# Kernel tuning notes

Measured on AMD Instinct MI355X. Metric: run time of the kernel, lower is better.

Reference implementation:

```python
import jax, jax.numpy as jnp
import numpy as np

BEV_H = 128; BEV_W = 128; HEADS = 8; POINTS = 4; NUM_LAYERS = 6
PC = (-51.2, -51.2, -5.0, 51.2, 51.2, 3.0)
EPS = 1e-5


def _layernorm(x, g, b):
    m = x.mean(-1, keepdims=True)
    v = x.var(-1, keepdims=True)
    return (x - m) * jax.lax.rsqrt(v + 1e-5) * g + b


def _bilinear(feat, loc):
    # feat: (H, W, D); loc: (..., 2) normalized xy in [0, 1]; zero padding outside.
    H, W = feat.shape[0], feat.shape[1]
    ix = loc[..., 0] * W - 0.5
    iy = loc[..., 1] * H - 0.5
    x0 = jnp.floor(ix); y0 = jnp.floor(iy)
    fx = ix - x0; fy = iy - y0
    out = 0.0
    for dx in (0, 1):
        for dy in (0, 1):
            xi = x0 + dx; yi = y0 + dy
            w = (fx if dx else 1.0 - fx) * (fy if dy else 1.0 - fy)
            m = (xi >= 0) & (xi < W) & (yi >= 0) & (yi < H)
            xi_c = jnp.clip(xi, 0, W - 1).astype(jnp.int32)
            yi_c = jnp.clip(yi, 0, H - 1).astype(jnp.int32)
            out = out + (w * m)[..., None] * feat[yi_c, xi_c]
    return out


def _deform_grid(q, value, H, W, ref, ow, ob, aw, ab):
    # Deformable attention over a (H, W) grid of values; q: (Nq, C), value: (H*W, C).
    Nq, C = q.shape
    hd = C // HEADS
    v = value.reshape(H, W, HEADS, hd).transpose(2, 0, 1, 3)            # (h, H, W, hd)
    off = (q @ ow + ob).reshape(Nq, HEADS, POINTS, 2)
    loc = ref[:, None, None, :] + off / jnp.array([W, H], q.dtype)      # (Nq, h, P, 2)
    attn = jax.nn.softmax((q @ aw + ab).reshape(Nq, HEADS, POINTS), axis=-1)
    sampled = jax.vmap(_bilinear)(v, loc.transpose(1, 0, 2, 3))         # (h, Nq, P, hd)
    return jnp.einsum('hnpd,nhp->nhd', sampled, attn).reshape(Nq, C)


def _sca(q, feats, ref_cam, valid, ow, ob, aw, ab):
    # Spatial cross-attention: feats (Ncam, h, Hf, Wf, hd), ref_cam (Ncam, Nq, P, 2),
    # valid (Ncam, Nq, P) float mask of in-frustum projections.
    Nq, C = q.shape
    Hf, Wf = feats.shape[2], feats.shape[3]
    off = (q @ ow + ob).reshape(Nq, HEADS, POINTS, 2)
    loc = ref_cam[:, None] + (off / jnp.array([Wf, Hf], q.dtype)).transpose(1, 0, 2, 3)[None]
    # loc: (Ncam, h, Nq, P, 2)
    attn = jax.nn.softmax((q @ aw + ab).reshape(Nq, HEADS, POINTS), axis=-1)
    sampled = jax.vmap(jax.vmap(_bilinear))(feats, loc)                 # (Ncam, h, Nq, P, hd)
    num = jnp.einsum('chnpd,nhp,cnp->nhd', sampled, attn, valid)
    cnt = jnp.maximum(valid.sum((0, 2)), 1.0)                           # (Nq,)
    return (num / cnt[:, None, None]).reshape(Nq, C)


def _forward(image_feats, camera_intrinsics, camera_extrinsics, prev_bev, bev_embed,
             tsa_vw, tsa_vb, tsa_ow, tsa_ob, tsa_aw, tsa_ab, tsa_pw, tsa_pb,
             sca_vw, sca_vb, sca_ow, sca_ob, sca_aw, sca_ab, sca_pw, sca_pb,
             ffn_w1, ffn_b1, ffn_w2, ffn_b2,
             ln1_g, ln1_b, ln2_g, ln2_b, ln3_g, ln3_b):
    Ncam, C, Hf, Wf = image_feats.shape
    hd = C // HEADS
    Nq = BEV_H * BEV_W
    dt = image_feats.dtype
    feats_flat = image_feats.transpose(0, 2, 3, 1).reshape(Ncam * Hf * Wf, C)

    # 2D reference points for temporal self-attention (each query's own cell).
    xs = (jnp.arange(BEV_W, dtype=dt) + 0.5) / BEV_W
    ys = (jnp.arange(BEV_H, dtype=dt) + 0.5) / BEV_H
    gx, gy = jnp.meshgrid(xs, ys)                                       # (H, W) each
    ref2d = jnp.stack([gx.reshape(-1), gy.reshape(-1)], -1)             # (Nq, 2)

    # 3D pillar reference points projected into each camera.
    xm = PC[0] + gx.reshape(-1) * (PC[3] - PC[0])
    ym = PC[1] + gy.reshape(-1) * (PC[4] - PC[1])
    zm = PC[2] + (jnp.arange(POINTS, dtype=dt) + 0.5) / POINTS * (PC[5] - PC[2])
    ref3d = jnp.stack([
        jnp.broadcast_to(xm[:, None], (Nq, POINTS)),
        jnp.broadcast_to(ym[:, None], (Nq, POINTS)),
        jnp.broadcast_to(zm[None, :], (Nq, POINTS)),
        jnp.ones((Nq, POINTS), dt)], -1)                                # (Nq, P, 4)
    ego2cam = jnp.linalg.inv(camera_extrinsics[0])                      # (Ncam, 4, 4)
    pcam = jnp.einsum('cij,npj->cnpi', ego2cam, ref3d)[..., :3]
    img = jnp.einsum('cij,cnpj->cnpi', camera_intrinsics[0], pcam)
    z = img[..., 2]
    un = img[..., 0] / (jnp.maximum(z, EPS) * Wf)
    vn = img[..., 1] / (jnp.maximum(z, EPS) * Hf)
    valid = ((z > EPS) & (un >= 0) & (un <= 1) & (vn >= 0) & (vn <= 1)).astype(dt)
    ref_cam = jnp.stack([un, vn], -1)                                   # (Ncam, Nq, P, 2)

    q = bev_embed                                                       # (Nq, C)
    prev = prev_bev[:, 0, :]                                            # (Nq, C), B = 1
    for l in range(NUM_LAYERS):
        # Temporal self-attention: deformable sampling from prev BEV + current BEV.
        v_prev = prev @ tsa_vw[l] + tsa_vb[l]
        v_cur = q @ tsa_vw[l] + tsa_vb[l]
        a = 0.5 * (_deform_grid(q, v_prev, BEV_H, BEV_W, ref2d, tsa_ow[l], tsa_ob[l], tsa_aw[l], tsa_ab[l])
                   + _deform_grid(q, v_cur, BEV_H, BEV_W, ref2d, tsa_ow[l], tsa_ob[l], tsa_aw[l], tsa_ab[l]))
        q = _layernorm(q + a @ tsa_pw[l] + tsa_pb[l], ln1_g[l], ln1_b[l])
        # Spatial cross-attention over multi-camera image features.
        v_img = (feats_flat @ sca_vw[l] + sca_vb[l]).reshape(Ncam, Hf, Wf, HEADS, hd).transpose(0, 3, 1, 2, 4)
        a = _sca(q, v_img, ref_cam, valid, sca_ow[l], sca_ob[l], sca_aw[l], sca_ab[l])
        q = _layernorm(q + a @ sca_pw[l] + sca_pb[l], ln2_g[l], ln2_b[l])
        # FFN
        a = jax.nn.relu(q @ ffn_w1[l] + ffn_b1[l]) @ ffn_w2[l] + ffn_b2[l]
        q = _layernorm(q + a, ln3_g[l], ln3_b[l])
    return q.T.reshape(1, C, BEV_H, BEV_W)


def setup_inputs() -> dict:
    key = jax.random.key(0)
    ks = iter(jax.random.split(key, 80))
    def nrm(shape, s=0.02):
        return jax.random.normal(next(ks), shape, jnp.float32) * s
    C, L, Ncam, Hf, Wf = 256, NUM_LAYERS, 6, 58, 100
    Nq = BEV_H * BEV_W
    HP, HP2 = HEADS * POINTS, HEADS * POINTS * 2
    # Structured nuScenes-like cameras: 6 yaws at 60 deg, intrinsics at feature-map scale.
    extr = np.zeros((1, Ncam, 4, 4), np.float32)
    for c in range(Ncam):
        t = c * np.pi / 3.0
        f = np.array([np.cos(t), np.sin(t), 0.0])
        xc = np.array([np.sin(t), -np.cos(t), 0.0])
        yc = np.array([0.0, 0.0, -1.0])
        extr[0, c, :3, :3] = np.stack([xc, yc, f], axis=1)
        extr[0, c, :3, 3] = 1.5 * f + np.array([0.0, 0.0, 1.5])
        extr[0, c, 3, 3] = 1.0
    intr = np.zeros((1, Ncam, 3, 3), np.float32)
    intr[0, :, 0, 0] = 80.0; intr[0, :, 1, 1] = 80.0
    intr[0, :, 0, 2] = Wf / 2.0; intr[0, :, 1, 2] = Hf / 2.0
    intr[0, :, 2, 2] = 1.0
    return {
        'image_feats': jax.random.normal(next(ks), (Ncam, C, Hf, Wf), jnp.float32),
        'camera_intrinsics': jnp.asarray(intr),
        'camera_extrinsics': jnp.asarray(extr),
        'prev_bev': jax.random.normal(next(ks), (Nq, 1, C), jnp.float32),
        'bev_embed': nrm((Nq, C)),
        'tsa_vw': nrm((L, C, C)), 'tsa_vb': jnp.zeros((L, C), jnp.float32),
        'tsa_ow': nrm((L, C, HP2)), 'tsa_ob': nrm((L, HP2), 2.0),
        'tsa_aw': nrm((L, C, HP)), 'tsa_ab': jnp.zeros((L, HP), jnp.float32),
        'tsa_pw': nrm((L, C, C)), 'tsa_pb': jnp.zeros((L, C), jnp.float32),
        'sca_vw': nrm((L, C, C)), 'sca_vb': jnp.zeros((L, C), jnp.float32),
        'sca_ow': nrm((L, C, HP2)), 'sca_ob': nrm((L, HP2), 2.0),
        'sca_aw': nrm((L, C, HP)), 'sca_ab': jnp.zeros((L, HP), jnp.float32),
        'sca_pw': nrm((L, C, C)), 'sca_pb': jnp.zeros((L, C), jnp.float32),
        'ffn_w1': nrm((L, C, 2 * C)), 'ffn_b1': jnp.zeros((L, 2 * C), jnp.float32),
        'ffn_w2': nrm((L, 2 * C, C)), 'ffn_b2': jnp.zeros((L, C), jnp.float32),
        'ln1_g': jnp.ones((L, C), jnp.float32), 'ln1_b': jnp.zeros((L, C), jnp.float32),
        'ln2_g': jnp.ones((L, C), jnp.float32), 'ln2_b': jnp.zeros((L, C), jnp.float32),
        'ln3_g': jnp.ones((L, C), jnp.float32), 'ln3_b': jnp.zeros((L, C), jnp.float32),
    }


def reference(image_feats, camera_intrinsics, camera_extrinsics, prev_bev, bev_embed,
              tsa_vw, tsa_vb, tsa_ow, tsa_ob, tsa_aw, tsa_ab, tsa_pw, tsa_pb,
              sca_vw, sca_vb, sca_ow, sca_ob, sca_aw, sca_ab, sca_pw, sca_pb,
              ffn_w1, ffn_b1, ffn_w2, ffn_b2,
              ln1_g, ln1_b, ln2_g, ln2_b, ln3_g, ln3_b):
    return _forward(image_feats, camera_intrinsics, camera_extrinsics, prev_bev, bev_embed,
                    tsa_vw, tsa_vb, tsa_ow, tsa_ob, tsa_aw, tsa_ab, tsa_pw, tsa_pb,
                    sca_vw, sca_vb, sca_ow, sca_ob, sca_aw, sca_ab, sca_pw, sca_pb,
                    ffn_w1, ffn_b1, ffn_w2, ffn_b2,
                    ln1_g, ln1_b, ln2_g, ln2_b, ln3_g, ln3_b)
```

## Files before the change

kernel.cpp:

```cpp
#include <hip/hip_runtime.h>
#include <hip/hip_bf16.h>
#include <math.h>

typedef __hip_bfloat16 bf16;

#define NQ      16384
#define CDIM    256
#define NHEADS  8
#define NPOINTS 4
#define NCAM    6
#define HF      58
#define WF      100
#define HWF     (HF*WF)
#define NFEAT   (NCAM*HWF)
#define HD      32
#define NLAYERS 6

typedef __attribute__((ext_vector_type(8))) short short8;
typedef __attribute__((ext_vector_type(4))) float floatx4;

__device__ __forceinline__ float toF(float x) { return x; }
__device__ __forceinline__ float toF(bf16 x) { return __bfloat162float(x); }
__device__ __forceinline__ void storeD(float* p, float v) { *p = v; }
__device__ __forceinline__ void storeD(bf16* p, float v) { *p = __float2bfloat16(v); }

__device__ __forceinline__ float bfLo(unsigned u) { return __uint_as_float(u << 16); }
__device__ __forceinline__ float bfHi(unsigned u) { return __uint_as_float(u & 0xffff0000u); }

__device__ __forceinline__ void gload_lds16(const bf16* g, bf16* l) {
    __builtin_amdgcn_global_load_lds(
        (const __attribute__((address_space(1))) void*)(g),
        (__attribute__((address_space(3))) void*)(l), 16, 0, 0);
}


template <typename DT, bool RELU, bool STAGE, bool ZF>
__global__ __launch_bounds__(256) void gemm_mfma(
    const bf16* __restrict__ A, const bf16* __restrict__ BT,
    const float* __restrict__ bias, DT* __restrict__ D,
    int M, int N, int K, size_t sB, size_t sBias, size_t sD)
{
    int z, bn, bm;
    if (ZF) {
        int nwg = gridDim.x;
        int logical = (blockIdx.x & 7) * (nwg >> 3) + (blockIdx.x >> 3);
        int idx = logical % (2 * NLAYERS);
        bm = (logical / (2 * NLAYERS)) * 128;
        z  = idx % NLAYERS;
        bn = (idx / NLAYERS) * 128;
    } else {
        z  = blockIdx.z;
        bn = blockIdx.x * 128;
        bm = blockIdx.y * 128;
    }
    BT += (size_t)z * sB;
    bias += (size_t)z * sBias;
    D += (size_t)z * sD;

    __shared__ bf16 smem[STAGE ? 128 * 136 : 128 * 64];
    bf16* As = smem;
    bf16* Bs = smem + 128 * 32;

    int tid = threadIdx.x;
    int lane = tid & 63, w = tid >> 6;
    int wm = w & 1, wn = w >> 1;
    int l15 = lane & 15, quad = lane >> 4;

    floatx4 acc[4][4];
#pragma unroll
    for (int i = 0; i < 4; i++)
#pragma unroll
        for (int j = 0; j < 4; j++)
            acc[i][j] = (floatx4){0.f, 0.f, 0.f, 0.f};

    int rsub = lane >> 2;
    int kc   = (((lane & 3) ^ ((rsub >> 1) & 3))) * 8;
    int sw   = (l15 >> 1) & 3;

    for (int k0 = 0; k0 < K; k0 += 32) {
#pragma unroll
        for (int h = 0; h < 2; h++) {
            int r0 = w * 32 + h * 16;
            int gm = bm + r0 + rsub;
            if (gm > M - 1) gm = M - 1;
            gload_lds16(A + (size_t)gm * K + k0 + kc, &As[r0 * 32]);
            gload_lds16(BT + (size_t)(bn + r0 + rsub) * K + k0 + kc, &Bs[r0 * 32]);
        }
        __syncthreads();

        short8 a[4], b[4];
#pragma unroll
        for (int i = 0; i < 4; i++)
            a[i] = *(const short8*)(&As[(wm * 64 + i * 16 + l15) * 32 + (quad ^ sw) * 8]);
#pragma unroll
        for (int j = 0; j < 4; j++)
            b[j] = *(const short8*)(&Bs[(wn * 64 + j * 16 + l15) * 32 + (quad ^ sw) * 8]);
#pragma unroll
        for (int i = 0; i < 4; i++)
#pragma unroll
            for (int j = 0; j < 4; j++)
                acc[i][j] = __builtin_amdgcn_mfma_f32_16x16x32_bf16(
                    a[i], b[j], acc[i][j], 0, 0, 0);
        __syncthreads();
    }

    if (STAGE) {
#pragma unroll
        for (int i = 0; i < 4; i++) {
#pragma unroll
            for (int j = 0; j < 4; j++) {
                int col = wn * 64 + j * 16 + l15;
                float bv = bias[bn + col];
#pragma unroll
                for (int r = 0; r < 4; r++) {
                    int row = wm * 64 + i * 16 + quad * 4 + r;
                    float v = acc[i][j][r] + bv;
                    if (RELU) v = fmaxf(v, 0.f);
                    smem[row * 136 + col] = __float2bfloat16(v);
                }
            }
        }
        __syncthreads();
        int lr0 = tid >> 4;
        int ck  = tid & 15;
#pragma unroll
        for (int pass = 0; pass < 8; pass++) {
            int lr = pass * 16 + lr0;
            int gm = bm + lr;
            if (gm < M) {
                uint4 v = *(const uint4*)(&smem[lr * 136 + ck * 8]);
                *(uint4*)((bf16*)D + (size_t)gm * N + bn + ck * 8) = v;
            }
        }
    } else {
#pragma unroll
        for (int i = 0; i < 4; i++) {
#pragma unroll
            for (int j = 0; j < 4; j++) {
                int col = bn + wn * 64 + j * 16 + l15;
                float bv = bias[col];
#pragma unroll
                for (int r = 0; r < 4; r++) {
                    int row = bm + wm * 64 + i * 16 + quad * 4 + r;
                    if (row < M) {
                        float v = acc[i][j][r] + bv;
                        if (RELU) v = fmaxf(v, 0.f);
                        storeD(&D[(size_t)row * N + col], v);
                    }
                }
            }
        }
    }
}

__global__ __launch_bounds__(256) void gemm_off(
    const bf16* __restrict__ A, const bf16* __restrict__ BT,
    const float* __restrict__ bias, float* __restrict__ D)
{
    __shared__ bf16 As[64 * 32];
    __shared__ bf16 Bs[64 * 32];

    int tid = threadIdx.x;
    int lane = tid & 63, w = tid >> 6;
    int l15 = lane & 15, quad = lane >> 4;
    int bm = blockIdx.y * 64, bn = blockIdx.x * 64;

    floatx4 acc[4];
#pragma unroll
    for (int j = 0; j < 4; j++)
        acc[j] = (floatx4){0.f, 0.f, 0.f, 0.f};

    int rsub = lane >> 2;
    int kc   = (((lane & 3) ^ ((rsub >> 1) & 3))) * 8;
    int sw   = (l15 >> 1) & 3;

    for (int k0 = 0; k0 < 256; k0 += 32) {
        gload_lds16(A + (size_t)(bm + w * 16 + rsub) * 256 + k0 + kc, &As[w * 16 * 32]);
        gload_lds16(BT + (size_t)(bn + w * 16 + rsub) * 256 + k0 + kc, &Bs[w * 16 * 32]);
        __syncthreads();

        short8 a = *(const short8*)(&As[(w * 16 + l15) * 32 + (quad ^ sw) * 8]);
        short8 b[4];
#pragma unroll
        for (int j = 0; j < 4; j++)
            b[j] = *(const short8*)(&Bs[(j * 16 + l15) * 32 + (quad ^ sw) * 8]);
#pragma unroll
        for (int j = 0; j < 4; j++)
            acc[j] = __builtin_amdgcn_mfma_f32_16x16x32_bf16(a, b[j], acc[j], 0, 0, 0);
        __syncthreads();
    }

#pragma unroll
    for (int j = 0; j < 4; j++) {
        int col = bn + j * 16 + l15;
        float bv = bias[col];
#pragma unroll
        for (int r = 0; r < 4; r++) {
            int row = bm + w * 16 + quad * 4 + r;
            D[(size_t)row * 128 + col] = acc[j][r] + bv;
        }
    }
}

__global__ __launch_bounds__(256) void gemm_tsa(
    const bf16* __restrict__ qmean, const bf16* __restrict__ qb,
    const bf16* __restrict__ BT, const float* __restrict__ bias,
    bf16* __restrict__ vgrid, float* __restrict__ offlog)
{
    int bn3 = blockIdx.x;
    int bm = blockIdx.y * 128;
    int bn = bn3 * 128;
    const bf16* A = (bn3 == 2) ? qb : qmean;

    __shared__ bf16 smem[128 * 136];
    bf16* As = smem;
    bf16* Bs = smem + 128 * 32;

    int tid = threadIdx.x;
    int lane = tid & 63, w = tid >> 6;
    int wm = w & 1, wn = w >> 1;
    int l15 = lane & 15, quad = lane >> 4;

    floatx4 acc[4][4];
#pragma unroll
    for (int i = 0; i < 4; i++)
#pragma unroll
        for (int j = 0; j < 4; j++)
            acc[i][j] = (floatx4){0.f, 0.f, 0.f, 0.f};

    int rsub = lane >> 2;
    int kc   = (((lane & 3) ^ ((rsub >> 1) & 3))) * 8;
    int sw   = (l15 >> 1) & 3;

    for (int k0 = 0; k0 < 256; k0 += 32) {
#pragma unroll
        for (int h = 0; h < 2; h++) {
            int r0 = w * 32 + h * 16;
            gload_lds16(A + (size_t)(bm + r0 + rsub) * 256 + k0 + kc, &As[r0 * 32]);
            gload_lds16(BT + (size_t)(bn + r0 + rsub) * 256 + k0 + kc, &Bs[r0 * 32]);
        }
        __syncthreads();

        short8 a[4], b[4];
#pragma unroll
        for (int i = 0; i < 4; i++)
            a[i] = *(const short8*)(&As[(wm * 64 + i * 16 + l15) * 32 + (quad ^ sw) * 8]);
#pragma unroll
        for (int j = 0; j < 4; j++)
            b[j] = *(const short8*)(&Bs[(wn * 64 + j * 16 + l15) * 32 + (quad ^ sw) * 8]);
#pragma unroll
        for (int i = 0; i < 4; i++)
#pragma unroll
            for (int j = 0; j < 4; j++)
                acc[i][j] = __builtin_amdgcn_mfma_f32_16x16x32_bf16(
                    a[i], b[j], acc[i][j], 0, 0, 0);
        __syncthreads();
    }

    if (bn3 < 2) {
#pragma unroll
        for (int i = 0; i < 4; i++) {
#pragma unroll
            for (int j = 0; j < 4; j++) {
                int col = wn * 64 + j * 16 + l15;
                float bv = bias[bn + col];
#pragma unroll
                for (int r = 0; r < 4; r++) {
                    int row = wm * 64 + i * 16 + quad * 4 + r;
                    smem[row * 136 + col] = __float2bfloat16(acc[i][j][r] + bv);
                }
            }
        }
        __syncthreads();
        int lr0 = tid >> 4;
        int ck  = tid & 15;
#pragma unroll
        for (int pass = 0; pass < 8; pass++) {
            int lr = pass * 16 + lr0;
            uint4 v = *(const uint4*)(&smem[lr * 136 + ck * 8]);
            *(uint4*)(vgrid + (size_t)(bm + lr) * 256 + bn + ck * 8) = v;
        }
    } else {
#pragma unroll
        for (int i = 0; i < 4; i++) {
#pragma unroll
            for (int j = 0; j < 4; j++) {
                int col = wn * 64 + j * 16 + l15;
                float bv = bias[256 + col];
#pragma unroll
                for (int r = 0; r < 4; r++) {
                    int row = bm + wm * 64 + i * 16 + quad * 4 + r;
                    offlog[(size_t)row * 128 + col] = acc[i][j][r] + bv;
                }
            }
        }
    }
}

template <bool QM>
__global__ __launch_bounds__(512) void gemm_ln(
    const bf16* __restrict__ A, const bf16* __restrict__ BT,
    const float* __restrict__ bias,
    bf16* __restrict__ qb,
    const float* __restrict__ g, const float* __restrict__ b,
    int K, const bf16* __restrict__ prevb, bf16* __restrict__ qmean)
{
    __shared__ bf16 As[64 * 32];
    __shared__ bf16 Bs[256 * 32];
    __shared__ float red[2][64][4];
    __shared__ float stats[2][64];

    int tid = threadIdx.x;
    int lane = tid & 63, w = tid >> 6;
    int wm = w & 1, wn = w >> 1;
    int l15 = lane & 15, quad = lane >> 4;
    int bm = blockIdx.x * 64;

    floatx4 acc[2][4];
#pragma unroll
    for (int i = 0; i < 2; i++)
#pragma unroll
        for (int j = 0; j < 4; j++)
            acc[i][j] = (floatx4){0.f, 0.f, 0.f, 0.f};

    int rsub = lane >> 2;
    int kc   = (((lane & 3) ^ ((rsub >> 1) & 3))) * 8;
    int sw   = (l15 >> 1) & 3;

    for (int k0 = 0; k0 < K; k0 += 32) {
#pragma unroll
        for (int h = 0; h < 2; h++) {
            int r0 = w * 32 + h * 16;
            gload_lds16(BT + (size_t)(r0 + rsub) * K + k0 + kc, &Bs[r0 * 32]);
        }
        if (w < 4)
            gload_lds16(A + (size_t)(bm + w * 16 + rsub) * K + k0 + kc,
                        &As[w * 16 * 32]);
        __syncthreads();

        short8 a[2], bfr[4];
#pragma unroll
        for (int i = 0; i < 2; i++)
            a[i] = *(const short8*)(&As[(wm * 32 + i * 16 + l15) * 32 + (quad ^ sw) * 8]);
#pragma unroll
        for (int j = 0; j < 4; j++)
            bfr[j] = *(const short8*)(&Bs[(wn * 64 + j * 16 + l15) * 32 + (quad ^ sw) * 8]);
#pragma unroll
        for (int i = 0; i < 2; i++)
#pragma unroll
            for (int j = 0; j < 4; j++)
                acc[i][j] = __builtin_amdgcn_mfma_f32_16x16x32_bf16(
                    a[i], bfr[j], acc[i][j], 0, 0, 0);
        __syncthreads();
    }

    float x[2][4][4];
#pragma unroll
    for (int i = 0; i < 2; i++) {
#pragma unroll
        for (int j = 0; j < 4; j++) {
            int col = wn * 64 + j * 16 + l15;
            float bv = bias[col];
#pragma unroll
            for (int r = 0; r < 4; r++) {
                int row = bm + wm * 32 + i * 16 + quad * 4 + r;
                x[i][j][r] = toF(qb[(size_t)row * CDIM + col]) + acc[i][j][r] + bv;
            }
        }
    }
#pragma unroll
    for (int i = 0; i < 2; i++) {
#pragma unroll
        for (int r = 0; r < 4; r++) {
            float s = x[i][0][r] + x[i][1][r] + x[i][2][r] + x[i][3][r];
            float sq = x[i][0][r] * x[i][0][r] + x[i][1][r] * x[i][1][r] +
                       x[i][2][r] * x[i][2][r] + x[i][3][r] * x[i][3][r];
#pragma unroll
            for (int m = 1; m < 16; m <<= 1) {
                s += __shfl_xor(s, m);
                sq += __shfl_xor(sq, m);
            }
            if (l15 == 0) {
                int rl = wm * 32 + i * 16 + quad * 4 + r;
                red[0][rl][wn] = s;
                red[1][rl][wn] = sq;
            }
        }
    }
    __syncthreads();
    if (tid < 64) {
        float s = red[0][tid][0] + red[0][tid][1] + red[0][tid][2] + red[0][tid][3];
        float sq = red[1][tid][0] + red[1][tid][1] + red[1][tid][2] + red[1][tid][3];
        float mean = s * (1.f / CDIM);
        float var = fmaxf(sq * (1.f / CDIM) - mean * mean, 0.f);
        stats[0][tid] = mean;
        stats[1][tid] = rsqrtf(var + 1e-5f);
    }
    __syncthreads();
#pragma unroll
    for (int i = 0; i < 2; i++) {
#pragma unroll
        for (int j = 0; j < 4; j++) {
            int col = wn * 64 + j * 16 + l15;
            float gc = g[col], bc = b[col];
#pragma unroll
            for (int r = 0; r < 4; r++) {
                int rl = wm * 32 + i * 16 + quad * 4 + r;
                int row = bm + rl;
                float y = (x[i][j][r] - stats[0][rl]) * stats[1][rl] * gc + bc;
                qb[(size_t)row * CDIM + col] = __float2bfloat16(y);
                if (QM)
                    qmean[(size_t)row * CDIM + col] = __float2bfloat16(
                        0.5f * (toF(prevb[(size_t)row * CDIM + col]) + y));
            }
        }
    }
}

__global__ __launch_bounds__(256) void qmean_kernel(
    const bf16* __restrict__ a, const bf16* __restrict__ b, bf16* __restrict__ o)
{
    int i = blockIdx.x * 256 + threadIdx.x;
    short8 va = ((const short8*)a)[i];
    short8 vb = ((const short8*)b)[i];
    short8 vo;
#pragma unroll
    for (int j = 0; j < 8; j++) {
        float fa = __uint_as_float(((unsigned)(unsigned short)va[j]) << 16);
        float fb = __uint_as_float(((unsigned)(unsigned short)vb[j]) << 16);
        union { bf16 h; short s; } u;
        u.h = __float2bfloat16(0.5f * (fa + fb));
        vo[j] = u.s;
    }
    ((short8*)o)[i] = vo;
}

__global__ void wt_cvt_kernel(const float* __restrict__ W, bf16* __restrict__ WT,
                              int K, int N)
{
    __shared__ float tile[32][33];
    int l = blockIdx.z;
    const float* Wl = W + (size_t)l * K * N;
    bf16* WTl = WT + (size_t)l * K * N;
    int k0 = blockIdx.x * 32, n0 = blockIdx.y * 32;
    int tx = threadIdx.x, ty = threadIdx.y;
    for (int i = 0; i < 32; i += 8)
        tile[ty + i][tx] = Wl[(size_t)(k0 + ty + i) * N + n0 + tx];
    __syncthreads();
    for (int i = 0; i < 32; i += 8)
        WTl[(size_t)(n0 + ty + i) * K + k0 + tx] = __float2bfloat16(tile[tx][ty + i]);
}

__global__ void pack_tsa_kernel(const float* __restrict__ vw, const float* __restrict__ vb,
                                const float* __restrict__ ow, const float* __restrict__ ob,
                                const float* __restrict__ aw, const float* __restrict__ ab,
                                bf16* __restrict__ WT, float* __restrict__ BIAS)
{
    int n = blockIdx.x;
    int l = blockIdx.y;
    int k = threadIdx.x;
    float v = 0.f;
    if (n < 256)      v = vw[((size_t)l * 256 + k) * 256 + n];
    else if (n < 320) v = ow[((size_t)l * 256 + k) * 64 + (n - 256)];
    else if (n < 352) v = aw[((size_t)l * 256 + k) * 32 + (n - 320)];
    WT[((size_t)l * 384 + n) * 256 + k] = __float2bfloat16(v);
    if (k == 0) {
        float bv = 0.f;
        if (n < 256)      bv = vb[l * 256 + n];
        else if (n < 320) bv = ob[l * 64 + (n - 256)];
        else if (n < 352) bv = ab[l * 32 + (n - 320)];
        BIAS[l * 384 + n] = bv;
    }
}

__global__ void pack_offattn_kernel(const float* __restrict__ ow, const float* __restrict__ ob,
                                    const float* __restrict__ aw, const float* __restrict__ ab,
                                    bf16* __restrict__ WT, float* __restrict__ BIAS)
{
    int l = blockIdx.y;
    int n = blockIdx.x;
    int k = threadIdx.x;
    float v = 0.f;
    if (n < 64)      v = ow[((size_t)l * 256 + k) * 64 + n];
    else if (n < 96) v = aw[((size_t)l * 256 + k) * 32 + (n - 64)];
    WT[((size_t)l * 128 + n) * 256 + k] = __float2bfloat16(v);
    if (k == 0) {
        float bv = 0.f;
        if (n < 64)      bv = ob[l * 64 + n];
        else if (n < 96) bv = ab[l * 32 + (n - 64)];
        BIAS[l * 128 + n] = bv;
    }
}

__global__ void feats_cvt_kernel(const float* __restrict__ in, bf16* __restrict__ outT)
{
    __shared__ float tile[32][33];
    int c = blockIdx.z;
    int r0 = blockIdx.x * 32, ch0 = blockIdx.y * 32;
    int tx = threadIdx.x, ty = threadIdx.y;
    for (int i = 0; i < 32; i += 8) {
        int r = r0 + tx, ch = ch0 + ty + i;
        tile[ty + i][tx] = (r < HWF) ? in[((size_t)c * CDIM + ch) * HWF + r] : 0.f;
    }
    __syncthreads();
    for (int i = 0; i < 32; i += 8) {
        int r = r0 + ty + i, ch = ch0 + tx;
        if (r < HWF)
            outT[((size_t)c * HWF + r) * CDIM + ch] = __float2bfloat16(tile[tx][ty + i]);
    }
}

__global__ __launch_bounds__(256) void cvt_bf16_kernel(const float* __restrict__ in,
                                                       bf16* __restrict__ out, int n)
{
    int i = blockIdx.x * 256 + threadIdx.x;
    if (i < n) out[i] = __float2bfloat16(in[i]);
}

__global__ void invert4_kernel(const float* __restrict__ extr, float* __restrict__ ego)
{
    int c = threadIdx.x;
    if (c >= NCAM) return;
    float a[4][8];
    for (int i = 0; i < 4; i++)
        for (int j = 0; j < 4; j++) {
            a[i][j] = extr[c * 16 + i * 4 + j];
            a[i][4 + j] = (i == j) ? 1.f : 0.f;
        }
    for (int col = 0; col < 4; col++) {
        int piv = col;
        float best = fabsf(a[col][col]);
        for (int r = col + 1; r < 4; r++) {
            float v = fabsf(a[r][col]);
            if (v > best) { best = v; piv = r; }
        }
        if (piv != col)
            for (int j = 0; j < 8; j++) {
                float t = a[col][j]; a[col][j] = a[piv][j]; a[piv][j] = t;
            }
        float inv = 1.f / a[col][col];
        for (int j = 0; j < 8; j++) a[col][j] *= inv;
        for (int r = 0; r < 4; r++) {
            if (r == col) continue;
            float f = a[r][col];
            for (int j = 0; j < 8; j++) a[r][j] -= f * a[col][j];
        }
    }
    for (int i = 0; i < 4; i++)
        for (int j = 0; j < 4; j++)
            ego[c * 16 + i * 4 + j] = a[i][4 + j];
}

__global__ __launch_bounds__(256) void refcam_compact_kernel(
    const float* __restrict__ ego, const float* __restrict__ intr,
    float4* __restrict__ entries, int* __restrict__ cnt)
{
    int n = blockIdx.x * 256 + threadIdx.x;
    if (n >= NQ) return;

    float gx = ((n & 127) + 0.5f) / 128.0f;
    float gy = ((n >> 7) + 0.5f) / 128.0f;
    float xm = -51.2f + gx * 102.4f;
    float ym = -51.2f + gy * 102.4f;

    float4* out = entries + (size_t)n * 24;
    int k = 0;
    for (int c = 0; c < NCAM; c++) {
        const float* E = ego + c * 16;
        const float* I = intr + c * 9;
#pragma unroll
        for (int p = 0; p < NPOINTS; p++) {
            float zm = -5.0f + (p + 0.5f) * 2.0f;
            float pc[3];
#pragma unroll
            for (int i = 0; i < 3; i++)
                pc[i] = E[i * 4 + 0] * xm + E[i * 4 + 1] * ym + E[i * 4 + 2] * zm + E[i * 4 + 3];
            float im[3];
#pragma unroll
            for (int i = 0; i < 3; i++)
                im[i] = I[i * 3 + 0] * pc[0] + I[i * 3 + 1] * pc[1] + I[i * 3 + 2] * pc[2];
            float z = im[2];
            float zc = fmaxf(z, 1e-5f);
            float un = im[0] / (zc * (float)WF);
            float vn = im[1] / (zc * (float)HF);
            if (z > 1e-5f && un >= 0.f && un <= 1.f && vn >= 0.f && vn <= 1.f) {
                out[k] = make_float4(un, vn, __int_as_float(c * 4 + p), 0.f);
                k++;
            }
        }
    }
    cnt[n] = k;
}

__global__ __launch_bounds__(256) void tsa_sample_kernel(
    const bf16* __restrict__ vgrid, const float* __restrict__ offlog,
    bf16* __restrict__ outA)
{
    int blk = blockIdx.x;
    int qq = (blk & 7) * 512 + (blk >> 3);
    int t = threadIdx.x;
    int n = qq * 4 + (t >> 6);
    int r = t & 63;
    int h = r >> 3;
    int dq = r & 7;
    int col = h * HD + dq * 4;

    const float* fl = offlog + (size_t)n * 128;
    const float* lg = fl + 64 + h * 4;
    float l0 = lg[0], l1 = lg[1], l2 = lg[2], l3 = lg[3];
    float mx = fmaxf(fmaxf(l0, l1), fmaxf(l2, l3));
    float e0 = expf(l0 - mx), e1 = expf(l1 - mx), e2 = expf(l2 - mx), e3 = expf(l3 - mx);
    float inv = 1.f / (e0 + e1 + e2 + e3);
    float w[4] = { e0 * inv, e1 * inv, e2 * inv, e3 * inv };

    const float* of = fl + h * 8;
    float rx = ((n & 127) + 0.5f) / 128.f;
    float ry = ((n >> 7) + 0.5f) / 128.f;

    float a0 = 0.f, a1 = 0.f, a2 = 0.f, a3 = 0.f;
#pragma unroll
    for (int p = 0; p < NPOINTS; p++) {
        float lx = rx + of[p * 2] * (1.f / 128.f);
        float ly = ry + of[p * 2 + 1] * (1.f / 128.f);
        float ix = lx * 128.f - 0.5f;
        float iy = ly * 128.f - 0.5f;
        float xf = floorf(ix), yf = floorf(iy);
        float fx = ix - xf, fy = iy - yf;
        int x0 = (int)xf, y0 = (int)yf;
#pragma unroll
        for (int dy = 0; dy < 2; dy++) {
            int yi = y0 + dy;
            if (yi < 0 || yi >= 128) continue;
            float wy = dy ? fy : 1.f - fy;
#pragma unroll
            for (int dx = 0; dx < 2; dx++) {
                int xi = x0 + dx;
                if (xi < 0 || xi >= 128) continue;
                float wgt = w[p] * wy * (dx ? fx : 1.f - fx);
                uint2 v = *(const uint2*)(vgrid + (size_t)(yi * 128 + xi) * 256 + col);
                a0 += wgt * bfLo(v.x);
                a1 += wgt * bfHi(v.x);
                a2 += wgt * bfLo(v.y);
                a3 += wgt * bfHi(v.y);
            }
        }
    }
    union { bf16 b[4]; uint2 u; } pk;
    pk.b[0] = __float2bfloat16(a0);
    pk.b[1] = __float2bfloat16(a1);
    pk.b[2] = __float2bfloat16(a2);
    pk.b[3] = __float2bfloat16(a3);
    *(uint2*)(outA + (size_t)n * CDIM + col) = pk.u;
}

__global__ __launch_bounds__(256) void sca_sample_kernel(
    const bf16* __restrict__ vimg, const float* __restrict__ offlog,
    const float4* __restrict__ entries, const int* __restrict__ cnt,
    bf16* __restrict__ outA)
{
    int blk = blockIdx.x;
    int qo = (blk & 7) * 256 + (blk >> 3);
    int t = threadIdx.x;
    int n = qo * 8 + (t >> 5);
    int r = t & 31;
    int h = r >> 2;
    int d8 = r & 3;
    int col = h * HD + d8 * 8;

    const float* fl = offlog + (size_t)n * 128;
    const float* lg = fl + 64 + h * 4;
    float l0 = lg[0], l1 = lg[1], l2 = lg[2], l3 = lg[3];
    float mx = fmaxf(fmaxf(l0, l1), fmaxf(l2, l3));
    float e0 = expf(l0 - mx), e1 = expf(l1 - mx), e2 = expf(l2 - mx), e3 = expf(l3 - mx);
    float inv = 1.f / (e0 + e1 + e2 + e3);
    float w[4] = { e0 * inv, e1 * inv, e2 * inv, e3 * inv };

    const float* of = fl + h * 8;
    float ox[4], oy[4];
#pragma unroll
    for (int p = 0; p < NPOINTS; p++) {
        ox[p] = of[p * 2] * (1.f / (float)WF);
        oy[p] = of[p * 2 + 1] * (1.f / (float)HF);
    }

    int ne = cnt[n];
    const float4* ent = entries + (size_t)n * 24;

    float a0 = 0.f, a1 = 0.f, a2 = 0.f, a3 = 0.f;
    float a4 = 0.f, a5 = 0.f, a6 = 0.f, a7 = 0.f;
    for (int e = 0; e < ne; e++) {
        float4 E = ent[e];
        int cp = __float_as_int(E.z);
        int c = cp >> 2, p = cp & 3;
        float lx = E.x + ox[p];
        float ly = E.y + oy[p];
        float ix = lx * (float)WF - 0.5f;
        float iy = ly * (float)HF - 0.5f;
        float xf = floorf(ix), yf = floorf(iy);
        float fx = ix - xf, fy = iy - yf;
        int x0 = (int)xf, y0 = (int)yf;
        float wp_ = w[p];
        const bf16* vb = vimg + (size_t)c * HWF * CDIM;
#pragma unroll
        for (int dy = 0; dy < 2; dy++) {
            int yi = y0 + dy;
            if (yi < 0 || yi >= HF) continue;
            float wy = dy ? fy : 1.f - fy;
#pragma unroll
            for (int dx = 0; dx < 2; dx++) {
                int xi = x0 + dx;
                if (xi < 0 || xi >= WF) continue;
                float wgt = wp_ * wy * (dx ? fx : 1.f - fx);
                uint4 u = *(const uint4*)(vb + (size_t)(yi * WF + xi) * CDIM + col);
                a0 += wgt * bfLo(u.x);
                a1 += wgt * bfHi(u.x);
                a2 += wgt * bfLo(u.y);
                a3 += wgt * bfHi(u.y);
                a4 += wgt * bfLo(u.z);
                a5 += wgt * bfHi(u.z);
                a6 += wgt * bfLo(u.w);
                a7 += wgt * bfHi(u.w);
            }
        }
    }
    float ic = 1.f / fmaxf((float)ne, 1.f);
    union { bf16 b[8]; uint4 u; } pk;
    pk.b[0] = __float2bfloat16(a0 * ic);
    pk.b[1] = __float2bfloat16(a1 * ic);
    pk.b[2] = __float2bfloat16(a2 * ic);
    pk.b[3] = __float2bfloat16(a3 * ic);
    pk.b[4] = __float2bfloat16(a4 * ic);
    pk.b[5] = __float2bfloat16(a5 * ic);
    pk.b[6] = __float2bfloat16(a6 * ic);
    pk.b[7] = __float2bfloat16(a7 * ic);
    *(uint4*)(outA + (size_t)n * CDIM + col) = pk.u;
}

__global__ void out_transpose_kernel(const bf16* __restrict__ qb, float* __restrict__ out)
{
    __shared__ float tile[32][33];
    int n0 = blockIdx.x * 32;
    int c0 = blockIdx.y * 32;
    int tx = threadIdx.x, ty = threadIdx.y;
    for (int i = 0; i < 32; i += 8)
        tile[ty + i][tx] = toF(qb[(size_t)(n0 + ty + i) * CDIM + c0 + tx]);
    __syncthreads();
    for (int i = 0; i < 32; i += 8)
        out[(size_t)(c0 + ty + i) * NQ + n0 + tx] = tile[tx][ty + i];
}

extern "C" void kernel_launch(void* const* d_in, const int* in_sizes, int n_in,
                              void* d_out, int out_size, void* d_ws, size_t ws_size,
                              hipStream_t stream)
{
    const float* image_feats = (const float*)d_in[0];
    const float* intr        = (const float*)d_in[1];
    const float* extr        = (const float*)d_in[2];
    const float* prev_bev    = (const float*)d_in[3];
    const float* bev_embed   = (const float*)d_in[4];
    const float* tsa_vw = (const float*)d_in[5];
    const float* tsa_vb = (const float*)d_in[6];
    const float* tsa_ow = (const float*)d_in[7];
    const float* tsa_ob = (const float*)d_in[8];
    const float* tsa_aw = (const float*)d_in[9];
    const float* tsa_ab = (const float*)d_in[10];
    const float* tsa_pw = (const float*)d_in[11];
    const float* tsa_pb = (const float*)d_in[12];
    const float* sca_vw = (const float*)d_in[13];
    const float* sca_vb = (const float*)d_in[14];
    const float* sca_ow = (const float*)d_in[15];
    const float* sca_ob = (const float*)d_in[16];
    const float* sca_aw = (const float*)d_in[17];
    const float* sca_ab = (const float*)d_in[18];
    const float* sca_pw = (const float*)d_in[19];
    const float* sca_pb = (const float*)d_in[20];
    const float* ffn_w1 = (const float*)d_in[21];
    const float* ffn_b1 = (const float*)d_in[22];
    const float* ffn_w2 = (const float*)d_in[23];
    const float* ffn_b2 = (const float*)d_in[24];
    const float* ln1_g  = (const float*)d_in[25];
    const float* ln1_b  = (const float*)d_in[26];
    const float* ln2_g  = (const float*)d_in[27];
    const float* ln2_b  = (const float*)d_in[28];
    const float* ln3_g  = (const float*)d_in[29];
    const float* ln3_b  = (const float*)d_in[30];

    char* wp = (char*)d_ws;
    auto alloc = [&](size_t bytes) -> void* {
        void* r = (void*)wp;
        wp += (bytes + 255) & ~(size_t)255;
        return r;
    };
    bf16*  prevbf = (bf16*) alloc((size_t)NQ * CDIM * 2);
    bf16*  qb     = (bf16*) alloc((size_t)NQ * CDIM * 2);
    bf16*  qmeanb = (bf16*) alloc((size_t)NQ * CDIM * 2);
    bf16*  attnA  = (bf16*) alloc((size_t)NQ * CDIM * 2);
    float* offlog = (float*)alloc((size_t)NQ * 128 * 4);
    float4* entries = (float4*)alloc((size_t)NQ * 24 * 16);
    int*   entcnt = (int*)  alloc((size_t)NQ * 4);
    float* ego    = (float*)alloc(128 * 4);
    bf16*  featsT = (bf16*) alloc((size_t)NFEAT * CDIM * 2);
    bf16*  pwT  = (bf16*)alloc((size_t)NLAYERS * 65536 * 2);
    bf16*  svwT = (bf16*)alloc((size_t)NLAYERS * 65536 * 2);
    bf16*  spwT = (bf16*)alloc((size_t)NLAYERS * 65536 * 2);
    bf16*  w1T  = (bf16*)alloc((size_t)NLAYERS * 131072 * 2);
    bf16*  w2T  = (bf16*)alloc((size_t)NLAYERS * 131072 * 2);
    bf16*  ptwT = (bf16*)alloc((size_t)NLAYERS * 384 * 256 * 2);
    float* ptb  = (float*)alloc((size_t)NLAYERS * 384 * 4);
    bf16*  sowT = (bf16*)alloc((size_t)NLAYERS * 32768 * 2);
    float* sobF = (float*)alloc((size_t)NLAYERS * 128 * 4);
    bf16*  vgrid = (bf16*)alloc((size_t)NQ * CDIM * 2);
    bf16*  vimg6 = (bf16*)alloc((size_t)NLAYERS * NFEAT * CDIM * 2);

    bf16* hidden = featsT;

    dim3 blk32(32, 8);

    cvt_bf16_kernel<<<(NQ * CDIM + 255) / 256, 256, 0, stream>>>(bev_embed, qb, NQ * CDIM);
    cvt_bf16_kernel<<<(NQ * CDIM + 255) / 256, 256, 0, stream>>>(prev_bev, prevbf, NQ * CDIM);
    qmean_kernel<<<NQ * CDIM / 8 / 256, 256, 0, stream>>>(prevbf, qb, qmeanb);
    invert4_kernel<<<1, 64, 0, stream>>>(extr, ego);
    refcam_compact_kernel<<<NQ / 256, 256, 0, stream>>>(ego, intr, entries, entcnt);
    {
        dim3 g((HWF + 31) / 32, CDIM / 32, NCAM);
        feats_cvt_kernel<<<g, blk32, 0, stream>>>(image_feats, featsT);
    }
    wt_cvt_kernel<<<dim3(8, 8,  NLAYERS), blk32, 0, stream>>>(tsa_pw, pwT,  256, 256);
    wt_cvt_kernel<<<dim3(8, 8,  NLAYERS), blk32, 0, stream>>>(sca_vw, svwT, 256, 256);
    wt_cvt_kernel<<<dim3(8, 8,  NLAYERS), blk32, 0, stream>>>(sca_pw, spwT, 256, 256);
    wt_cvt_kernel<<<dim3(8, 16, NLAYERS), blk32, 0, stream>>>(ffn_w1, w1T, 256, 512);
    wt_cvt_kernel<<<dim3(16, 8, NLAYERS), blk32, 0, stream>>>(ffn_w2, w2T, 512, 256);
    pack_tsa_kernel<<<dim3(384, NLAYERS), 256, 0, stream>>>(
        tsa_vw, tsa_vb, tsa_ow, tsa_ob, tsa_aw, tsa_ab, ptwT, ptb);
    pack_offattn_kernel<<<dim3(128, NLAYERS), 256, 0, stream>>>(
        sca_ow, sca_ob, sca_aw, sca_ab, sowT, sobF);
    gemm_mfma<bf16, false, true, true><<<dim3(2 * NLAYERS * 272), 256, 0, stream>>>(
        featsT, svwT, sca_vb, vimg6, NFEAT, CDIM, CDIM,
        65536, 256, (size_t)NFEAT * CDIM);

    for (int l = 0; l < NLAYERS; l++) {
        gemm_tsa<<<dim3(3, NQ / 128), 256, 0, stream>>>(
            qmeanb, qb, ptwT + (size_t)l * 98304, ptb + l * 384, vgrid, offlog);
        tsa_sample_kernel<<<NQ / 4, 256, 0, stream>>>(vgrid, offlog, attnA);
        gemm_ln<false><<<NQ / 64, 512, 0, stream>>>(
            attnA, pwT + (size_t)l * 65536, tsa_pb + l * CDIM,
            qb, ln1_g + l * CDIM, ln1_b + l * CDIM, CDIM, nullptr, nullptr);

        gemm_off<<<dim3(2, NQ / 64), 256, 0, stream>>>(
            qb, sowT + (size_t)l * 32768, sobF + l * 128, offlog);
        sca_sample_kernel<<<NQ / 8, 256, 0, stream>>>(
            vimg6 + (size_t)l * NFEAT * CDIM, offlog, entries, entcnt, attnA);
        gemm_ln<false><<<NQ / 64, 512, 0, stream>>>(
            attnA, spwT + (size_t)l * 65536, sca_pb + l * CDIM,
            qb, ln2_g + l * CDIM, ln2_b + l * CDIM, CDIM, nullptr, nullptr);

        gemm_mfma<bf16, true, true, false><<<dim3(4, NQ / 128, 1), 256, 0, stream>>>(
            qb, w1T + (size_t)l * 131072, ffn_b1 + l * 512, hidden, NQ, 512, CDIM, 0, 0, 0);
        if (l < NLAYERS - 1)
            gemm_ln<true><<<NQ / 64, 512, 0, stream>>>(
                hidden, w2T + (size_t)l * 131072, ffn_b2 + l * CDIM,
                qb, ln3_g + l * CDIM, ln3_b + l * CDIM, 512, prevbf, qmeanb);
        else
            gemm_ln<false><<<NQ / 64, 512, 0, stream>>>(
                hidden, w2T + (size_t)l * 131072, ffn_b2 + l * CDIM,
                qb, ln3_g + l * CDIM, ln3_b + l * CDIM, 512, nullptr, nullptr);
    }

    {
        dim3 g(NQ / 32, CDIM / 32);
        out_transpose_kernel<<<g, blk32, 0, stream>>>(qb, (float*)d_out);
    }
}
```

Baseline: 933.6 us.

## Fuse FFN up-projection, ReLU, down-projection and LayerNorm into one kernel

Replaces the separate FFN first GEMM (which wrote a 16384x512 bf16 hidden tensor to global memory) and the GEMM+LayerNorm kernel with one kernel per 64-row tile. The ReLU hidden activations stay in a 64KB swizzled shared-memory buffer and feed the second GEMM directly. This removes the hidden-tensor write and read and one launch per layer. The cost is roughly 100KB of LDS per block, which limits occupancy to about one block per CU, and each block reloads the full W1 and W2.

After: 897.3 us. -3.9%, faster.

```diff
diff --git a/kernel.cpp b/kernel.cpp
--- a/kernel.cpp
+++ b/kernel.cpp
@@ -361,6 +361,185 @@
         for (int j = 0; j < 4; j++) {
             int col = wn * 64 + j * 16 + l15;
             float bv = bias[col];
+#pragma unroll
+            for (int r = 0; r < 4; r++) {
+                int row = bm + wm * 32 + i * 16 + quad * 4 + r;
+                x[i][j][r] = toF(qb[(size_t)row * CDIM + col]) + acc[i][j][r] + bv;
+            }
+        }
+    }
+#pragma unroll
+    for (int i = 0; i < 2; i++) {
+#pragma unroll
+        for (int r = 0; r < 4; r++) {
+            float s = x[i][0][r] + x[i][1][r] + x[i][2][r] + x[i][3][r];
+            float sq = x[i][0][r] * x[i][0][r] + x[i][1][r] * x[i][1][r] +
+                       x[i][2][r] * x[i][2][r] + x[i][3][r] * x[i][3][r];
+#pragma unroll
+            for (int m = 1; m < 16; m <<= 1) {
+                s += __shfl_xor(s, m);
+                sq += __shfl_xor(sq, m);
+            }
+            if (l15 == 0) {
+                int rl = wm * 32 + i * 16 + quad * 4 + r;
+                red[0][rl][wn] = s;
+                red[1][rl][wn] = sq;
+            }
+        }
+    }
+    __syncthreads();
+    if (tid < 64) {
+        float s = red[0][tid][0] + red[0][tid][1] + red[0][tid][2] + red[0][tid][3];
+        float sq = red[1][tid][0] + red[1][tid][1] + red[1][tid][2] + red[1][tid][3];
+        float mean = s * (1.f / CDIM);
+        float var = fmaxf(sq * (1.f / CDIM) - mean * mean, 0.f);
+        stats[0][tid] = mean;
+        stats[1][tid] = rsqrtf(var + 1e-5f);
+    }
+    __syncthreads();
+#pragma unroll
+    for (int i = 0; i < 2; i++) {
+#pragma unroll
+        for (int j = 0; j < 4; j++) {
+            int col = wn * 64 + j * 16 + l15;
+            float gc = g[col], bc = b[col];
+#pragma unroll
+            for (int r = 0; r < 4; r++) {
+                int rl = wm * 32 + i * 16 + quad * 4 + r;
+                int row = bm + rl;
+                float y = (x[i][j][r] - stats[0][rl]) * stats[1][rl] * gc + bc;
+                qb[(size_t)row * CDIM + col] = __float2bfloat16(y);
+                if (QM)
+                    qmean[(size_t)row * CDIM + col] = __float2bfloat16(
+                        0.5f * (toF(prevb[(size_t)row * CDIM + col]) + y));
+            }
+        }
+    }
+}
+
+template <bool QM>
+__global__ __launch_bounds__(512) void ffn_fused(
+    const bf16* __restrict__ W1T,
+    const float* __restrict__ b1,
+    const bf16* __restrict__ W2T,
+    const float* __restrict__ b2,
+    bf16* __restrict__ qb,
+    const float* __restrict__ g, const float* __restrict__ b,
+    const bf16* __restrict__ prevb, bf16* __restrict__ qmean)
+{
+    __shared__ bf16 Hs[64 * 512];
+    __shared__ bf16 As[64 * 32];
+    __shared__ bf16 Bs[512 * 32];
+    __shared__ float red[2][64][4];
+    __shared__ float stats[2][64];
+
+    int tid = threadIdx.x;
+    int lane = tid & 63, w = tid >> 6;
+    int l15 = lane & 15, quad = lane >> 4;
+    int bm = blockIdx.x * 64;
+
+    int rsub = lane >> 2;
+    int kc   = (((lane & 3) ^ ((rsub >> 1) & 3))) * 8;
+    int sw   = (l15 >> 1) & 3;
+
+    {
+        floatx4 acc[4][4];
+#pragma unroll
+        for (int i = 0; i < 4; i++)
+#pragma unroll
+            for (int j = 0; j < 4; j++)
+                acc[i][j] = (floatx4){0.f, 0.f, 0.f, 0.f};
+
+        for (int k0 = 0; k0 < 256; k0 += 32) {
+#pragma unroll
+            for (int h = 0; h < 4; h++) {
+                int r0 = w * 64 + h * 16;
+                gload_lds16(W1T + (size_t)(r0 + rsub) * 256 + k0 + kc, &Bs[r0 * 32]);
+            }
+            if (w < 4)
+                gload_lds16(qb + (size_t)(bm + w * 16 + rsub) * 256 + k0 + kc,
+                            &As[w * 16 * 32]);
+            __syncthreads();
+
+            short8 a[4], bfr[4];
+#pragma unroll
+            for (int i = 0; i < 4; i++)
+                a[i] = *(const short8*)(&As[(i * 16 + l15) * 32 + (quad ^ sw) * 8]);
+#pragma unroll
+            for (int j = 0; j < 4; j++)
+                bfr[j] = *(const short8*)(&Bs[(w * 64 + j * 16 + l15) * 32 + (quad ^ sw) * 8]);
+#pragma unroll
+            for (int i = 0; i < 4; i++)
+#pragma unroll
+                for (int j = 0; j < 4; j++)
+                    acc[i][j] = __builtin_amdgcn_mfma_f32_16x16x32_bf16(
+                        a[i], bfr[j], acc[i][j], 0, 0, 0);
+            __syncthreads();
+        }
+
+#pragma unroll
+        for (int j = 0; j < 4; j++) {
+            int col = w * 64 + j * 16 + l15;
+            float bv = b1[col];
+            int chunk = col >> 3;
+            int coff = col & 7;
+#pragma unroll
+            for (int i = 0; i < 4; i++) {
+#pragma unroll
+                for (int r = 0; r < 4; r++) {
+                    int row = i * 16 + quad * 4 + r;
+                    float v = fmaxf(acc[i][j][r] + bv, 0.f);
+                    Hs[row * 512 + ((chunk ^ (row & 15)) << 3) + coff] =
+                        __float2bfloat16(v);
+                }
+            }
+        }
+    }
+    __syncthreads();
+
+    int wm = w & 1, wn = w >> 1;
+
+    floatx4 acc[2][4];
+#pragma unroll
+    for (int i = 0; i < 2; i++)
+#pragma unroll
+        for (int j = 0; j < 4; j++)
+            acc[i][j] = (floatx4){0.f, 0.f, 0.f, 0.f};
+
+    for (int k0 = 0; k0 < 512; k0 += 32) {
+#pragma unroll
+        for (int h = 0; h < 2; h++) {
+            int r0 = w * 32 + h * 16;
+            gload_lds16(W2T + (size_t)(r0 + rsub) * 512 + k0 + kc, &Bs[r0 * 32]);
+        }
+        __syncthreads();
+
+        short8 a[2], bfr[4];
+        int kch = (k0 >> 3) + quad;
+#pragma unroll
+        for (int i = 0; i < 2; i++) {
+            int row = wm * 32 + i * 16 + l15;
+            a[i] = *(const short8*)(&Hs[row * 512 + ((kch ^ l15) << 3)]);
+        }
+#pragma unroll
+        for (int j = 0; j < 4; j++)
+            bfr[j] = *(const short8*)(&Bs[(wn * 64 + j * 16 + l15) * 32 + (quad ^ sw) * 8]);
+#pragma unroll
+        for (int i = 0; i < 2; i++)
+#pragma unroll
+            for (int j = 0; j < 4; j++)
+                acc[i][j] = __builtin_amdgcn_mfma_f32_16x16x32_bf16(
+                    a[i], bfr[j], acc[i][j], 0, 0, 0);
+        __syncthreads();
+    }
+
+    float x[2][4][4];
+#pragma unroll
+    for (int i = 0; i < 2; i++) {
+#pragma unroll
+        for (int j = 0; j < 4; j++) {
+            int col = wn * 64 + j * 16 + l15;
+            float bv = b2[col];
 #pragma unroll
             for (int r = 0; r < 4; r++) {
                 int row = bm + wm * 32 + i * 16 + quad * 4 + r;
@@ -812,8 +991,6 @@
     bf16*  vgrid = (bf16*)alloc((size_t)NQ * CDIM * 2);
     bf16*  vimg6 = (bf16*)alloc((size_t)NLAYERS * NFEAT * CDIM * 2);
 
-    bf16* hidden = featsT;
-
     dim3 blk32(32, 8);
 
     cvt_bf16_kernel<<<(NQ * CDIM + 255) / 256, 256, 0, stream>>>(bev_embed, qb, NQ * CDIM);
@@ -854,16 +1031,16 @@
             attnA, spwT + (size_t)l * 65536, sca_pb + l * CDIM,
             qb, ln2_g + l * CDIM, ln2_b + l * CDIM, CDIM, nullptr, nullptr);
 
-        gemm_mfma<bf16, true, true, false><<<dim3(4, NQ / 128, 1), 256, 0, stream>>>(
-            qb, w1T + (size_t)l * 131072, ffn_b1 + l * 512, hidden, NQ, 512, CDIM, 0, 0, 0);
         if (l < NLAYERS - 1)
-            gemm_ln<true><<<NQ / 64, 512, 0, stream>>>(
-                hidden, w2T + (size_t)l * 131072, ffn_b2 + l * CDIM,
-                qb, ln3_g + l * CDIM, ln3_b + l * CDIM, 512, prevbf, qmeanb);
+            ffn_fused<true><<<NQ / 64, 512, 0, stream>>>(
+                w1T + (size_t)l * 131072, ffn_b1 + l * 512,
+                w2T + (size_t)l * 131072, ffn_b2 + l * CDIM,
+                qb, ln3_g + l * CDIM, ln3_b + l * CDIM, prevbf, qmeanb);
         else
-            gemm_ln<false><<<NQ / 64, 512, 0, stream>>>(
-                hidden, w2T + (size_t)l * 131072, ffn_b2 + l * CDIM,
-                qb, ln3_g + l * CDIM, ln3_b + l * CDIM, 512, nullptr, nullptr);
+            ffn_fused<false><<<NQ / 64, 512, 0, stream>>>(
+                w1T + (size_t)l * 131072, ffn_b1 + l * 512,
+                w2T + (size_t)l * 131072, ffn_b2 + l * CDIM,
+                qb, ln3_g + l * CDIM, ln3_b + l * CDIM, nullptr, nullptr);
     }
 
     {
```
